# Kernel optimization log

Hardware: AMD Instinct MI355X
Metric: run time of the kernel (lower is better)

The kernel has to match this reference:

```python
import jax, jax.numpy as jnp
import numpy as np

N_NODES = 50000
N_EDGES = 500000
N_GRAPHS = 256
D_IN, D_H1, D_H2, D_H3, D_OUT = 768, 256, 128, 64, 2


def _glorot(key, shape):
    fan_in, fan_out = shape[1], shape[0]
    lim = float(np.sqrt(6.0 / (fan_in + fan_out)))
    return jax.random.uniform(key, shape, jnp.float32, -lim, lim)


def setup_inputs() -> dict:
    key = jax.random.key(0)
    ks = jax.random.split(key, 12)
    x = jax.random.normal(ks[0], (N_NODES, D_IN), jnp.float32)
    edge_index = jax.random.randint(ks[1], (2, N_EDGES), 0, N_NODES, jnp.int64)
    batch = jnp.sort(jax.random.randint(ks[2], (N_NODES,), 0, N_GRAPHS, jnp.int64))
    return {
        "x": x,
        "edge_index": edge_index,
        "batch": batch,
        # SAGEConv1: out = lin_l(mean_aggr) + lin_r(x); bias only on lin_l (PyG default)
        "W1_l": _glorot(ks[3], (D_H1, D_IN)),
        "b1_l": jnp.zeros((D_H1,), jnp.float32),
        "W1_r": _glorot(ks[4], (D_H1, D_IN)),
        # SAGEConv2
        "W2_l": _glorot(ks[5], (D_H2, D_H1)),
        "b2_l": jnp.zeros((D_H2,), jnp.float32),
        "W2_r": _glorot(ks[6], (D_H2, D_H1)),
        # MLP head
        "W3": _glorot(ks[7], (D_H3, D_H2)),
        "b3": jnp.zeros((D_H3,), jnp.float32),
        "W4": _glorot(ks[8], (D_OUT, D_H3)),
        "b4": jnp.zeros((D_OUT,), jnp.float32),
    }


def _sage_conv(x, src, dst, deg_inv, W_l, b_l, W_r):
    # mean aggregation of neighbor features: scatter-add then divide by in-degree
    aggr = jax.ops.segment_sum(x[src], dst, num_segments=N_NODES)  # [N, d]
    aggr = aggr * deg_inv[:, None]
    return aggr @ W_l.T + b_l + x @ W_r.T


def reference(x, edge_index, batch, W1_l, b1_l, W1_r, W2_l, b2_l, W2_r, W3, b3, W4, b4):
    src, dst = edge_index[0], edge_index[1]
    deg = jax.ops.segment_sum(jnp.ones((N_EDGES,), x.dtype), dst, num_segments=N_NODES)
    deg_inv = jnp.where(deg > 0, 1.0 / jnp.maximum(deg, 1.0), 0.0)

    h = jax.nn.relu(_sage_conv(x, src, dst, deg_inv, W1_l, b1_l, W1_r))
    h = jax.nn.relu(_sage_conv(h, src, dst, deg_inv, W2_l, b2_l, W2_r))

    # global_mean_pool over graph ids
    pooled = jax.ops.segment_sum(h, batch, num_segments=N_GRAPHS)  # [G, 128]
    cnt = jax.ops.segment_sum(jnp.ones((N_NODES,), h.dtype), batch, num_segments=N_GRAPHS)
    pooled = pooled / jnp.maximum(cnt, 1.0)[:, None]

    # dropout is identity in eval mode
    h = pooled @ W3.T + b3
    h = h @ W4.T + b4
    return jax.nn.softmax(h, axis=-1)
```

## Files before the change

kernel.cpp:

```cpp
#include <hip/hip_runtime.h>
#include <cstdint>
#include <cstddef>

#define N_NODES 50000
#define N_EDGES 500000
#define N_GRAPHS 256
#define D_IN 768
#define D_H1 256
#define D_H2 128

typedef __attribute__((ext_vector_type(8))) __bf16 bf16x8;
typedef __attribute__((ext_vector_type(4))) float f32x4;

__device__ __forceinline__ float bf2f(uint32_t u) {
    union { uint32_t i; float f; } v; v.i = u << 16; return v.f;
}
__device__ __forceinline__ uint32_t f2bf(float f) {
    union { float f; uint32_t i; } v; v.f = f;
    uint32_t u = v.i;
    return (u + 0x7FFFu + ((u >> 16) & 1u)) >> 16;
}

__global__ void k_packA(const float* __restrict__ in, uint16_t* __restrict__ out,
                        int nchunks, int KT, int K) {
    int c = blockIdx.x * 256 + threadIdx.x;
    if (c >= nchunks) return;
    int l = c & 63, t = c >> 6;
    int kt = t % KT, mt = t / KT;
    int fr = l & 15, fq = l >> 4;
    const float* p = in + (size_t)(mt * 16 + fr) * K + kt * 32 + fq * 8;
    float4 u = *(const float4*)p, v = *(const float4*)(p + 4);
    uint4 o;
    o.x = f2bf(u.x) | (f2bf(u.y) << 16);
    o.y = f2bf(u.z) | (f2bf(u.w) << 16);
    o.z = f2bf(v.x) | (f2bf(v.y) << 16);
    o.w = f2bf(v.z) | (f2bf(v.w) << 16);
    *(uint4*)(out + (size_t)c * 8) = o;
}

__global__ void k_packW(const float* __restrict__ inL, const float* __restrict__ inR,
                        uint16_t* __restrict__ out, int rowsL, int nchunks, int KT, int K) {
    int c = blockIdx.x * 256 + threadIdx.x;
    if (c >= nchunks) return;
    int l = c & 63, t = c >> 6;
    int kt = t % KT, mt = t / KT;
    int fr = l & 15, fq = l >> 4;
    int row = mt * 16 + fr;
    const float* src = (row < rowsL) ? (inL + (size_t)row * K) : (inR + (size_t)(row - rowsL) * K);
    const float* p = src + kt * 32 + fq * 8;
    float4 u = *(const float4*)p, v = *(const float4*)(p + 4);
    uint4 o;
    o.x = f2bf(u.x) | (f2bf(u.y) << 16);
    o.y = f2bf(u.z) | (f2bf(u.w) << 16);
    o.z = f2bf(v.x) | (f2bf(v.y) << 16);
    o.w = f2bf(v.z) | (f2bf(v.w) << 16);
    *(uint4*)(out + (size_t)c * 8) = o;
}

__global__ void k_hist(const int* __restrict__ dst, int* __restrict__ deg, int n) {
    int e = blockIdx.x * blockDim.x + threadIdx.x;
    if (e < n) atomicAdd(&deg[dst[e]], 1);
}

__global__ void k_scan1(const int* __restrict__ deg, int* __restrict__ row_ex,
                        int* __restrict__ bsum, int n) {
    __shared__ int buf[256];
    int t = threadIdx.x, i = blockIdx.x * 256 + t;
    int v = (i < n) ? deg[i] : 0;
    buf[t] = v; __syncthreads();
    for (int off = 1; off < 256; off <<= 1) {
        int u = (t >= off) ? buf[t - off] : 0;
        __syncthreads(); buf[t] += u; __syncthreads();
    }
    if (i < n) row_ex[i] = buf[t] - v;
    if (t == 255) bsum[blockIdx.x] = buf[255];
}
__global__ void k_scan2(const int* __restrict__ bsum, int* __restrict__ boff, int nb) {
    __shared__ int buf[256];
    int t = threadIdx.x;
    int v = (t < nb) ? bsum[t] : 0;
    buf[t] = v; __syncthreads();
    for (int off = 1; off < 256; off <<= 1) {
        int u = (t >= off) ? buf[t - off] : 0;
        __syncthreads(); buf[t] += u; __syncthreads();
    }
    if (t < nb) boff[t] = buf[t] - v;
}
__global__ void k_scan3(const int* __restrict__ deg, const int* __restrict__ boff,
                        int* __restrict__ row_start, float* __restrict__ deg_inv, int n) {
    int i = blockIdx.x * 256 + threadIdx.x;
    if (i < n) {
        row_start[i] += boff[blockIdx.x];
        int d = deg[i];
        deg_inv[i] = (d > 0) ? (1.0f / (float)d) : 0.0f;
    }
    if (blockIdx.x == 0 && threadIdx.x == 0) row_start[n] = N_EDGES;
}

__global__ void k_fill(const int* __restrict__ src, const int* __restrict__ dst,
                       const int* __restrict__ row_start, int* __restrict__ cursor,
                       int* __restrict__ csr_src, int n) {
    int e = blockIdx.x * blockDim.x + threadIdx.x;
    if (e < n) {
        int d = dst[e];
        int pos = row_start[d] + atomicAdd(&cursor[d], 1);
        csr_src[pos] = src[e];
    }
}

__global__ __launch_bounds__(256, 2) void k_mgemm(
    const uint16_t* __restrict__ Ap, const uint16_t* __restrict__ Bp,
    uint16_t* __restrict__ C, int M, int N, int KT)
{
    const int tid = threadIdx.x;
    const int wave = tid >> 6, lane = tid & 63;
    const int fr = lane & 15, fq = lane >> 4;
    const int bn = blockIdx.x * 256, bm = blockIdx.y * 128;
    const int wm = (wave >> 1) * 64, wn = (wave & 1) * 128;
    const int mtiles = (M + 15) >> 4;

    const bf16x8* ap[4];
    const bf16x8* bp[8];
    #pragma unroll
    for (int mi = 0; mi < 4; ++mi) {
        int mt = ((bm + wm) >> 4) + mi;
        if (mt > mtiles - 1) mt = mtiles - 1;
        ap[mi] = (const bf16x8*)Ap + (size_t)mt * KT * 64 + lane;
    }
    #pragma unroll
    for (int ni = 0; ni < 8; ++ni) {
        int nt = ((bn + wn) >> 4) + ni;
        bp[ni] = (const bf16x8*)Bp + (size_t)nt * KT * 64 + lane;
    }

    f32x4 acc[4][8] = {};
    bf16x8 a0[4], b0[8], a1[4], b1[8];

    auto lA = [&](int kt, bf16x8* d) {
        #pragma unroll
        for (int mi = 0; mi < 4; ++mi) d[mi] = ap[mi][kt * 64];
    };
    auto lB = [&](int kt, bf16x8* d) {
        #pragma unroll
        for (int ni = 0; ni < 8; ++ni) d[ni] = bp[ni][kt * 64];
    };
    auto step = [&](bf16x8* a, bf16x8* b) {
        #pragma unroll
        for (int mi = 0; mi < 4; ++mi)
            #pragma unroll
            for (int ni = 0; ni < 8; ++ni)
                acc[mi][ni] = __builtin_amdgcn_mfma_f32_16x16x32_bf16(
                    a[mi], b[ni], acc[mi][ni], 0, 0, 0);
    };

    lA(0, a0); lB(0, b0);
    for (int ks = 0; ks < KT; ks += 2) {
        lA(ks + 1, a1); lB(ks + 1, b1);
        step(a0, b0);
        if (ks + 2 < KT) { lA(ks + 2, a0); lB(ks + 2, b0); }
        step(a1, b1);
    }

    #pragma unroll
    for (int mi = 0; mi < 4; ++mi) {
        #pragma unroll
        for (int r = 0; r < 4; ++r) {
            int row = bm + wm + mi * 16 + fq * 4 + r;
            if (row >= M) continue;
            #pragma unroll
            for (int ni = 0; ni < 8; ++ni) {
                int col = bn + wn + ni * 16 + fr;
                C[(size_t)row * N + col] = (uint16_t)f2bf(acc[mi][ni][r]);
            }
        }
    }
}

__global__ __launch_bounds__(256) void k_agg1(
    const uint16_t* __restrict__ y, const int* __restrict__ row_start,
    const int* __restrict__ csr, const float* __restrict__ deg_inv,
    const float* __restrict__ bias, uint16_t* __restrict__ h1p)
{
    int node = blockIdx.x * 8 + (threadIdx.x >> 5);
    if (node >= N_NODES) return;
    int c = threadIdx.x & 31;
    int s = row_start[node], e = row_start[node + 1];
    float a[8] = {};
    int p = s;
    for (; p + 1 < e; p += 2) {
        uint4 t0 = *(const uint4*)(y + (size_t)csr[p] * 512 + c * 8);
        uint4 t1 = *(const uint4*)(y + (size_t)csr[p + 1] * 512 + c * 8);
        a[0] += bf2f(t0.x & 0xFFFF) + bf2f(t1.x & 0xFFFF);
        a[1] += bf2f(t0.x >> 16)    + bf2f(t1.x >> 16);
        a[2] += bf2f(t0.y & 0xFFFF) + bf2f(t1.y & 0xFFFF);
        a[3] += bf2f(t0.y >> 16)    + bf2f(t1.y >> 16);
        a[4] += bf2f(t0.z & 0xFFFF) + bf2f(t1.z & 0xFFFF);
        a[5] += bf2f(t0.z >> 16)    + bf2f(t1.z >> 16);
        a[6] += bf2f(t0.w & 0xFFFF) + bf2f(t1.w & 0xFFFF);
        a[7] += bf2f(t0.w >> 16)    + bf2f(t1.w >> 16);
    }
    if (p < e) {
        uint4 t0 = *(const uint4*)(y + (size_t)csr[p] * 512 + c * 8);
        a[0] += bf2f(t0.x & 0xFFFF); a[1] += bf2f(t0.x >> 16);
        a[2] += bf2f(t0.y & 0xFFFF); a[3] += bf2f(t0.y >> 16);
        a[4] += bf2f(t0.z & 0xFFFF); a[5] += bf2f(t0.z >> 16);
        a[6] += bf2f(t0.w & 0xFFFF); a[7] += bf2f(t0.w >> 16);
    }
    float w = deg_inv[node];
    uint4 tx = *(const uint4*)(y + (size_t)node * 512 + 256 + c * 8);
    float4 b0 = *(const float4*)(bias + c * 8);
    float4 b1 = *(const float4*)(bias + c * 8 + 4);
    float v0 = fmaxf(a[0] * w + bf2f(tx.x & 0xFFFF) + b0.x, 0.f);
    float v1 = fmaxf(a[1] * w + bf2f(tx.x >> 16)    + b0.y, 0.f);
    float v2 = fmaxf(a[2] * w + bf2f(tx.y & 0xFFFF) + b0.z, 0.f);
    float v3 = fmaxf(a[3] * w + bf2f(tx.y >> 16)    + b0.w, 0.f);
    float v4 = fmaxf(a[4] * w + bf2f(tx.z & 0xFFFF) + b1.x, 0.f);
    float v5 = fmaxf(a[5] * w + bf2f(tx.z >> 16)    + b1.y, 0.f);
    float v6 = fmaxf(a[6] * w + bf2f(tx.w & 0xFFFF) + b1.z, 0.f);
    float v7 = fmaxf(a[7] * w + bf2f(tx.w >> 16)    + b1.w, 0.f);
    uint4 o;
    o.x = f2bf(v0) | (f2bf(v1) << 16);
    o.y = f2bf(v2) | (f2bf(v3) << 16);
    o.z = f2bf(v4) | (f2bf(v5) << 16);
    o.w = f2bf(v6) | (f2bf(v7) << 16);
    uint32_t addr = (((node >> 4) * 8 + (c >> 2)) * 64 + (c & 3) * 16 + (node & 15));
    *(uint4*)(h1p + (size_t)addr * 8) = o;
}

__global__ __launch_bounds__(256) void k_agg2(
    const uint16_t* __restrict__ y, const int* __restrict__ row_start,
    const int* __restrict__ csr, const float* __restrict__ deg_inv,
    const float* __restrict__ bias, float* __restrict__ out)
{
    int node = blockIdx.x * 4 + (threadIdx.x >> 6);
    if (node >= N_NODES) return;
    int lane = threadIdx.x & 63;
    int s = row_start[node], e = row_start[node + 1];
    float a0 = 0.f, a1 = 0.f;
    int p = s;
    for (; p + 1 < e; p += 2) {
        uint32_t t0 = *(const uint32_t*)(y + (size_t)csr[p] * 256 + lane * 2);
        uint32_t t1 = *(const uint32_t*)(y + (size_t)csr[p + 1] * 256 + lane * 2);
        a0 += bf2f(t0 & 0xFFFF) + bf2f(t1 & 0xFFFF);
        a1 += bf2f(t0 >> 16)    + bf2f(t1 >> 16);
    }
    if (p < e) {
        uint32_t t0 = *(const uint32_t*)(y + (size_t)csr[p] * 256 + lane * 2);
        a0 += bf2f(t0 & 0xFFFF);
        a1 += bf2f(t0 >> 16);
    }
    float w = deg_inv[node];
    uint32_t tx = *(const uint32_t*)(y + (size_t)node * 256 + 128 + lane * 2);
    float2 b = *(const float2*)(bias + lane * 2);
    float2 o;
    o.x = fmaxf(a0 * w + bf2f(tx & 0xFFFF) + b.x, 0.f);
    o.y = fmaxf(a1 * w + bf2f(tx >> 16)    + b.y, 0.f);
    *(float2*)(out + (size_t)node * 128 + lane * 2) = o;
}

__global__ void k_pool(const float* __restrict__ h2, const int* __restrict__ batch,
                       float* __restrict__ pooled)
{
    int g = blockIdx.x;
    __shared__ int s_lo, s_hi;
    if (threadIdx.x == 0) {
        int lo = 0, hi = N_NODES;
        while (lo < hi) { int m = (lo + hi) >> 1; if (batch[m] < g) lo = m + 1; else hi = m; }
        s_lo = lo;
        int lo2 = lo, hi2 = N_NODES;
        while (lo2 < hi2) { int m = (lo2 + hi2) >> 1; if (batch[m] < g + 1) lo2 = m + 1; else hi2 = m; }
        s_hi = lo2;
    }
    __syncthreads();
    int dim = threadIdx.x;
    float sum = 0.f;
    for (int i = s_lo; i < s_hi; ++i) sum += h2[(size_t)i * D_H2 + dim];
    int cnt = s_hi - s_lo;
    pooled[g * D_H2 + dim] = sum / (float)(cnt > 0 ? cnt : 1);
}

__global__ void k_head(const float* __restrict__ pooled, const float* __restrict__ W3,
                       const float* __restrict__ b3, const float* __restrict__ W4,
                       const float* __restrict__ b4, float* __restrict__ out)
{
    int g = blockIdx.x;
    int j = threadIdx.x;
    __shared__ float p[128];
    __shared__ float hid[64];
    __shared__ float logit[2];
    p[j] = pooled[g * 128 + j];
    p[j + 64] = pooled[g * 128 + 64 + j];
    __syncthreads();
    float s = b3[j];
    #pragma unroll 4
    for (int k = 0; k < 128; ++k) s = fmaf(p[k], W3[j * 128 + k], s);
    hid[j] = s;
    __syncthreads();
    if (j < 2) {
        float l = b4[j];
        for (int k = 0; k < 64; ++k) l = fmaf(hid[k], W4[j * 64 + k], l);
        logit[j] = l;
    }
    __syncthreads();
    if (j == 0) {
        float m = fmaxf(logit[0], logit[1]);
        float e0 = expf(logit[0] - m), e1 = expf(logit[1] - m);
        float inv = 1.0f / (e0 + e1);
        out[g * 2 + 0] = e0 * inv;
        out[g * 2 + 1] = e1 * inv;
    }
}

extern "C" void kernel_launch(void* const* d_in, const int* in_sizes, int n_in,
                              void* d_out, int out_size, void* d_ws, size_t ws_size,
                              hipStream_t stream)
{
    const float* x     = (const float*)d_in[0];
    const int*   ei    = (const int*)d_in[1];
    const int*   batch = (const int*)d_in[2];
    const float* W1l   = (const float*)d_in[3];
    const float* b1l   = (const float*)d_in[4];
    const float* W1r   = (const float*)d_in[5];
    const float* W2l   = (const float*)d_in[6];
    const float* b2l   = (const float*)d_in[7];
    const float* W2r   = (const float*)d_in[8];
    const float* W3    = (const float*)d_in[9];
    const float* b3    = (const float*)d_in[10];
    const float* W4    = (const float*)d_in[11];
    const float* b4    = (const float*)d_in[12];
    float* out = (float*)d_out;

    const int* e_src = ei;
    const int* e_dst = ei + N_EDGES;

    char* ws = (char*)d_ws;
    size_t off = 0;
    auto alloc = [&](size_t bytes) -> void* {
        void* p = ws + off;
        off = (off + bytes + 255) & ~(size_t)255;
        return p;
    };
    int*      deg       = (int*)alloc((size_t)N_NODES * 4);
    int*      row_start = (int*)alloc((size_t)(N_NODES + 1) * 4);
    int*      cursor    = (int*)alloc((size_t)N_NODES * 4);
    int*      csr_src   = (int*)alloc((size_t)N_EDGES * 4);
    float*    deg_inv   = (float*)alloc((size_t)N_NODES * 4);
    int*      bsum      = (int*)alloc(256 * 4);
    int*      boff      = (int*)alloc(256 * 4);
    float*    pooled    = (float*)alloc((size_t)N_GRAPHS * D_H2 * 4);
    uint16_t* W1p       = (uint16_t*)alloc((size_t)512 * 768 * 2);
    uint16_t* W2p       = (uint16_t*)alloc((size_t)256 * 256 * 2);
    uint16_t* xp        = (uint16_t*)alloc((size_t)N_NODES * D_IN * 2);
    uint16_t* y1        = (uint16_t*)alloc((size_t)N_NODES * 512 * 2);
    uint16_t* h1p       = (uint16_t*)alloc((size_t)N_NODES * 256 * 2);

    uint16_t* y2 = xp;
    float*    h2 = (float*)(xp + (size_t)N_NODES * 256);

    hipMemsetAsync(deg, 0, (size_t)N_NODES * 4, stream);
    hipMemsetAsync(cursor, 0, (size_t)N_NODES * 4, stream);

    k_hist<<<(N_EDGES + 255) / 256, 256, 0, stream>>>(e_dst, deg, N_EDGES);
    int nscan = (N_NODES + 255) / 256;
    k_scan1<<<nscan, 256, 0, stream>>>(deg, row_start, bsum, N_NODES);
    k_scan2<<<1, 256, 0, stream>>>(bsum, boff, nscan);
    k_scan3<<<nscan, 256, 0, stream>>>(deg, boff, row_start, deg_inv, N_NODES);
    k_fill<<<(N_EDGES + 255) / 256, 256, 0, stream>>>(e_src, e_dst, row_start, cursor, csr_src, N_EDGES);

    int ncA = 3125 * 24 * 64;
    k_packA<<<(ncA + 255) / 256, 256, 0, stream>>>(x, xp, ncA, 24, 768);
    int ncW1 = 32 * 24 * 64;
    k_packW<<<(ncW1 + 255) / 256, 256, 0, stream>>>(W1l, W1r, W1p, 256, ncW1, 24, 768);
    int ncW2 = 16 * 8 * 64;
    k_packW<<<(ncW2 + 255) / 256, 256, 0, stream>>>(W2l, W2r, W2p, 128, ncW2, 8, 256);

    dim3 g1(2, (N_NODES + 127) / 128);
    k_mgemm<<<g1, 256, 0, stream>>>(xp, W1p, y1, N_NODES, 512, 24);
    k_agg1<<<(N_NODES + 7) / 8, 256, 0, stream>>>(y1, row_start, csr_src, deg_inv, b1l, h1p);

    dim3 g2(1, (N_NODES + 127) / 128);
    k_mgemm<<<g2, 256, 0, stream>>>(h1p, W2p, y2, N_NODES, 256, 8);
    k_agg2<<<(N_NODES + 3) / 4, 256, 0, stream>>>(y2, row_start, csr_src, deg_inv, b2l, h2);

    k_pool<<<N_GRAPHS, 128, 0, stream>>>(h2, batch, pooled);
    k_head<<<N_GRAPHS, 64, 0, stream>>>(pooled, W3, b3, W4, b4, out);
}
```

Baseline: 529.7 us.

## Fuse preprocessing kernels, use decoupled-lookback scan, fuse pooling into aggregation

Merges the x/W packing and the degree histogram into one multi-role kernel, replaces the three-kernel scan with a single-pass decoupled-lookback scan, and folds global mean pooling into the second aggregation via atomics. The mean division moves into the head kernel, and one memset now covers all zeroed buffers. This removes several launches and drops the h2 write and reread. The cost is float atomic contention on pooled, where one graph holds about 200 nodes, plus a lookback scan that depends on all its blocks being resident at once.

```diff
diff --git a/kernel.cpp b/kernel.cpp
--- a/kernel.cpp
+++ b/kernel.cpp
@@ -21,15 +21,9 @@
     return (u + 0x7FFFu + ((u >> 16) & 1u)) >> 16;
 }
 
-__global__ void k_packA(const float* __restrict__ in, uint16_t* __restrict__ out,
-                        int nchunks, int KT, int K) {
-    int c = blockIdx.x * 256 + threadIdx.x;
-    if (c >= nchunks) return;
-    int l = c & 63, t = c >> 6;
-    int kt = t % KT, mt = t / KT;
-    int fr = l & 15, fq = l >> 4;
-    const float* p = in + (size_t)(mt * 16 + fr) * K + kt * 32 + fq * 8;
-    float4 u = *(const float4*)p, v = *(const float4*)(p + 4);
+__device__ __forceinline__ void pack_chunk(const float* __restrict__ src_row,
+                                           uint16_t* __restrict__ out, int c) {
+    float4 u = *(const float4*)src_row, v = *(const float4*)(src_row + 4);
     uint4 o;
     o.x = f2bf(u.x) | (f2bf(u.y) << 16);
     o.y = f2bf(u.z) | (f2bf(u.w) << 16);
@@ -38,63 +32,85 @@
     *(uint4*)(out + (size_t)c * 8) = o;
 }
 
-__global__ void k_packW(const float* __restrict__ inL, const float* __restrict__ inR,
-                        uint16_t* __restrict__ out, int rowsL, int nchunks, int KT, int K) {
-    int c = blockIdx.x * 256 + threadIdx.x;
-    if (c >= nchunks) return;
-    int l = c & 63, t = c >> 6;
-    int kt = t % KT, mt = t / KT;
-    int fr = l & 15, fq = l >> 4;
-    int row = mt * 16 + fr;
-    const float* src = (row < rowsL) ? (inL + (size_t)row * K) : (inR + (size_t)(row - rowsL) * K);
-    const float* p = src + kt * 32 + fq * 8;
-    float4 u = *(const float4*)p, v = *(const float4*)(p + 4);
-    uint4 o;
-    o.x = f2bf(u.x) | (f2bf(u.y) << 16);
-    o.y = f2bf(u.z) | (f2bf(u.w) << 16);
-    o.z = f2bf(v.x) | (f2bf(v.y) << 16);
-    o.w = f2bf(v.z) | (f2bf(v.w) << 16);
-    *(uint4*)(out + (size_t)c * 8) = o;
-}
-
-__global__ void k_hist(const int* __restrict__ dst, int* __restrict__ deg, int n) {
-    int e = blockIdx.x * blockDim.x + threadIdx.x;
-    if (e < n) atomicAdd(&deg[dst[e]], 1);
-}
-
-__global__ void k_scan1(const int* __restrict__ deg, int* __restrict__ row_ex,
-                        int* __restrict__ bsum, int n) {
+#define PA_BLK 18750
+#define HI_BLK 1954
+#define PW1_BLK 192
+#define PW2_BLK 32
+__global__ __launch_bounds__(256) void k_combo(
+    const float* __restrict__ x, uint16_t* __restrict__ xp,
+    const int* __restrict__ dst, int* __restrict__ deg,
+    const float* __restrict__ W1l, const float* __restrict__ W1r, uint16_t* __restrict__ W1p,
+    const float* __restrict__ W2l, const float* __restrict__ W2r, uint16_t* __restrict__ W2p)
+{
+    int b = blockIdx.x, tid = threadIdx.x;
+    if (b < PA_BLK) {
+        int c = b * 256 + tid;
+        int l = c & 63, t = c >> 6;
+        int kt = t % 24, mt = t / 24;
+        int fr = l & 15, fq = l >> 4;
+        pack_chunk(x + (size_t)(mt * 16 + fr) * 768 + kt * 32 + fq * 8, xp, c);
+    } else if (b < PA_BLK + HI_BLK) {
+        int e = (b - PA_BLK) * 256 + tid;
+        if (e < N_EDGES) atomicAdd(&deg[dst[e]], 1);
+    } else if (b < PA_BLK + HI_BLK + PW1_BLK) {
+        int c = (b - PA_BLK - HI_BLK) * 256 + tid;
+        int l = c & 63, t = c >> 6;
+        int kt = t % 24, mt = t / 24;
+        int fr = l & 15, fq = l >> 4;
+        int row = mt * 16 + fr;
+        const float* src = (row < 256) ? (W1l + (size_t)row * 768)
+                                       : (W1r + (size_t)(row - 256) * 768);
+        pack_chunk(src + kt * 32 + fq * 8, W1p, c);
+    } else {
+        int c = (b - PA_BLK - HI_BLK - PW1_BLK) * 256 + tid;
+        int l = c & 63, t = c >> 6;
+        int kt = t % 8, mt = t / 8;
+        int fr = l & 15, fq = l >> 4;
+        int row = mt * 16 + fr;
+        const float* src = (row < 128) ? (W2l + (size_t)row * 256)
+                                       : (W2r + (size_t)(row - 128) * 256);
+        pack_chunk(src + kt * 32 + fq * 8, W2p, c);
+    }
+}
+
+__global__ __launch_bounds__(256) void k_scan(
+    const int* __restrict__ deg, unsigned long long* __restrict__ desc,
+    int* __restrict__ row_start, float* __restrict__ deg_inv, int n)
+{
     __shared__ int buf[256];
-    int t = threadIdx.x, i = blockIdx.x * 256 + t;
+    __shared__ int s_prefix;
+    int bid = blockIdx.x, t = threadIdx.x;
+    int i = bid * 256 + t;
     int v = (i < n) ? deg[i] : 0;
     buf[t] = v; __syncthreads();
     for (int off = 1; off < 256; off <<= 1) {
         int u = (t >= off) ? buf[t - off] : 0;
         __syncthreads(); buf[t] += u; __syncthreads();
     }
-    if (i < n) row_ex[i] = buf[t] - v;
-    if (t == 255) bsum[blockIdx.x] = buf[255];
-}
-__global__ void k_scan2(const int* __restrict__ bsum, int* __restrict__ boff, int nb) {
-    __shared__ int buf[256];
-    int t = threadIdx.x;
-    int v = (t < nb) ? bsum[t] : 0;
-    buf[t] = v; __syncthreads();
-    for (int off = 1; off < 256; off <<= 1) {
-        int u = (t >= off) ? buf[t - off] : 0;
-        __syncthreads(); buf[t] += u; __syncthreads();
-    }
-    if (t < nb) boff[t] = buf[t] - v;
-}
-__global__ void k_scan3(const int* __restrict__ deg, const int* __restrict__ boff,
-                        int* __restrict__ row_start, float* __restrict__ deg_inv, int n) {
-    int i = blockIdx.x * 256 + threadIdx.x;
+    if (t == 0) {
+        unsigned long long total = (unsigned long long)(unsigned)buf[255];
+        __hip_atomic_store(&desc[bid], (1ull << 32) | total,
+                           __ATOMIC_RELEASE, __HIP_MEMORY_SCOPE_AGENT);
+        unsigned long long run = 0;
+        for (int j = bid - 1; j >= 0; --j) {
+            unsigned long long d;
+            do {
+                d = __hip_atomic_load(&desc[j], __ATOMIC_ACQUIRE, __HIP_MEMORY_SCOPE_AGENT);
+            } while ((d >> 32) == 0);
+            run += (d & 0xFFFFFFFFull);
+            if ((d >> 32) == 2) break;
+        }
+        __hip_atomic_store(&desc[bid], (2ull << 32) | (run + total),
+                           __ATOMIC_RELEASE, __HIP_MEMORY_SCOPE_AGENT);
+        s_prefix = (int)run;
+    }
+    __syncthreads();
+    int ex = s_prefix + buf[t] - v;
     if (i < n) {
-        row_start[i] += boff[blockIdx.x];
-        int d = deg[i];
-        deg_inv[i] = (d > 0) ? (1.0f / (float)d) : 0.0f;
-    }
-    if (blockIdx.x == 0 && threadIdx.x == 0) row_start[n] = N_EDGES;
+        row_start[i] = ex;
+        deg_inv[i] = (v > 0) ? (1.0f / (float)v) : 0.0f;
+        if (i == n - 1) row_start[n] = ex + v;
+    }
 }
 
 __global__ void k_fill(const int* __restrict__ src, const int* __restrict__ dst,
@@ -227,10 +243,11 @@
     *(uint4*)(h1p + (size_t)addr * 8) = o;
 }
 
-__global__ __launch_bounds__(256) void k_agg2(
+__global__ __launch_bounds__(256) void k_agg2pool(
     const uint16_t* __restrict__ y, const int* __restrict__ row_start,
     const int* __restrict__ csr, const float* __restrict__ deg_inv,
-    const float* __restrict__ bias, float* __restrict__ out)
+    const float* __restrict__ bias, const int* __restrict__ batch,
+    float* __restrict__ pooled)
 {
     int node = blockIdx.x * 4 + (threadIdx.x >> 6);
     if (node >= N_NODES) return;
@@ -252,44 +269,35 @@
     float w = deg_inv[node];
     uint32_t tx = *(const uint32_t*)(y + (size_t)node * 256 + 128 + lane * 2);
     float2 b = *(const float2*)(bias + lane * 2);
-    float2 o;
-    o.x = fmaxf(a0 * w + bf2f(tx & 0xFFFF) + b.x, 0.f);
-    o.y = fmaxf(a1 * w + bf2f(tx >> 16)    + b.y, 0.f);
-    *(float2*)(out + (size_t)node * 128 + lane * 2) = o;
-}
-
-__global__ void k_pool(const float* __restrict__ h2, const int* __restrict__ batch,
-                       float* __restrict__ pooled)
-{
-    int g = blockIdx.x;
-    __shared__ int s_lo, s_hi;
-    if (threadIdx.x == 0) {
-        int lo = 0, hi = N_NODES;
-        while (lo < hi) { int m = (lo + hi) >> 1; if (batch[m] < g) lo = m + 1; else hi = m; }
-        s_lo = lo;
-        int lo2 = lo, hi2 = N_NODES;
-        while (lo2 < hi2) { int m = (lo2 + hi2) >> 1; if (batch[m] < g + 1) lo2 = m + 1; else hi2 = m; }
-        s_hi = lo2;
-    }
-    __syncthreads();
-    int dim = threadIdx.x;
-    float sum = 0.f;
-    for (int i = s_lo; i < s_hi; ++i) sum += h2[(size_t)i * D_H2 + dim];
-    int cnt = s_hi - s_lo;
-    pooled[g * D_H2 + dim] = sum / (float)(cnt > 0 ? cnt : 1);
-}
-
-__global__ void k_head(const float* __restrict__ pooled, const float* __restrict__ W3,
-                       const float* __restrict__ b3, const float* __restrict__ W4,
-                       const float* __restrict__ b4, float* __restrict__ out)
+    float h0 = fmaxf(a0 * w + bf2f(tx & 0xFFFF) + b.x, 0.f);
+    float h1 = fmaxf(a1 * w + bf2f(tx >> 16)    + b.y, 0.f);
+    int g = batch[node];
+    atomicAdd(&pooled[g * 128 + lane * 2], h0);
+    atomicAdd(&pooled[g * 128 + lane * 2 + 1], h1);
+}
+
+__global__ void k_head(const float* __restrict__ pooled, const int* __restrict__ batch,
+                       const float* __restrict__ W3, const float* __restrict__ b3,
+                       const float* __restrict__ W4, const float* __restrict__ b4,
+                       float* __restrict__ out)
 {
     int g = blockIdx.x;
     int j = threadIdx.x;
     __shared__ float p[128];
     __shared__ float hid[64];
     __shared__ float logit[2];
-    p[j] = pooled[g * 128 + j];
-    p[j + 64] = pooled[g * 128 + 64 + j];
+    __shared__ float s_inv;
+    if (j == 0) {
+        int lo = 0, hi = N_NODES;
+        while (lo < hi) { int m = (lo + hi) >> 1; if (batch[m] < g) lo = m + 1; else hi = m; }
+        int lo2 = lo, hi2 = N_NODES;
+        while (lo2 < hi2) { int m = (lo2 + hi2) >> 1; if (batch[m] < g + 1) lo2 = m + 1; else hi2 = m; }
+        int cnt = lo2 - lo;
+        s_inv = 1.0f / (float)(cnt > 0 ? cnt : 1);
+    }
+    __syncthreads();
+    p[j]      = pooled[g * 128 + j] * s_inv;
+    p[j + 64] = pooled[g * 128 + 64 + j] * s_inv;
     __syncthreads();
     float s = b3[j];
     #pragma unroll 4
@@ -341,13 +349,13 @@
         return p;
     };
     int*      deg       = (int*)alloc((size_t)N_NODES * 4);
+    int*      cursor    = (int*)alloc((size_t)N_NODES * 4);
+    float*    pooled    = (float*)alloc((size_t)N_GRAPHS * D_H2 * 4);
+    unsigned long long* desc = (unsigned long long*)alloc(196 * 8);
+    size_t zero_span = off;
     int*      row_start = (int*)alloc((size_t)(N_NODES + 1) * 4);
-    int*      cursor    = (int*)alloc((size_t)N_NODES * 4);
     int*      csr_src   = (int*)alloc((size_t)N_EDGES * 4);
     float*    deg_inv   = (float*)alloc((size_t)N_NODES * 4);
-    int*      bsum      = (int*)alloc(256 * 4);
-    int*      boff      = (int*)alloc(256 * 4);
-    float*    pooled    = (float*)alloc((size_t)N_GRAPHS * D_H2 * 4);
     uint16_t* W1p       = (uint16_t*)alloc((size_t)512 * 768 * 2);
     uint16_t* W2p       = (uint16_t*)alloc((size_t)256 * 256 * 2);
     uint16_t* xp        = (uint16_t*)alloc((size_t)N_NODES * D_IN * 2);
@@ -355,33 +363,18 @@
     uint16_t* h1p       = (uint16_t*)alloc((size_t)N_NODES * 256 * 2);
 
     uint16_t* y2 = xp;
-    float*    h2 = (float*)(xp + (size_t)N_NODES * 256);
-
-    hipMemsetAsync(deg, 0, (size_t)N_NODES * 4, stream);
-    hipMemsetAsync(cursor, 0, (size_t)N_NODES * 4, stream);
-
-    k_hist<<<(N_EDGES + 255) / 256, 256, 0, stream>>>(e_dst, deg, N_EDGES);
-    int nscan = (N_NODES + 255) / 256;
-    k_scan1<<<nscan, 256, 0, stream>>>(deg, row_start, bsum, N_NODES);
-    k_scan2<<<1, 256, 0, stream>>>(bsum, boff, nscan);
-    k_scan3<<<nscan, 256, 0, stream>>>(deg, boff, row_start, deg_inv, N_NODES);
+
+    hipMemsetAsync(deg, 0, zero_span, stream);
+
+    k_combo<<<PA_BLK + HI_BLK + PW1_BLK + PW2_BLK, 256, 0, stream>>>(
+        x, xp, e_dst, deg, W1l, W1r, W1p, W2l, W2r, W2p);
+    k_scan<<<196, 256, 0, stream>>>(deg, desc, row_start, deg_inv, N_NODES);
     k_fill<<<(N_EDGES + 255) / 256, 256, 0, stream>>>(e_src, e_dst, row_start, cursor, csr_src, N_EDGES);
-
-    int ncA = 3125 * 24 * 64;
-    k_packA<<<(ncA + 255) / 256, 256, 0, stream>>>(x, xp, ncA, 24, 768);
-    int ncW1 = 32 * 24 * 64;
-    k_packW<<<(ncW1 + 255) / 256, 256, 0, stream>>>(W1l, W1r, W1p, 256, ncW1, 24, 768);
-    int ncW2 = 16 * 8 * 64;
-    k_packW<<<(ncW2 + 255) / 256, 256, 0, stream>>>(W2l, W2r, W2p, 128, ncW2, 8, 256);
-
     dim3 g1(2, (N_NODES + 127) / 128);
     k_mgemm<<<g1, 256, 0, stream>>>(xp, W1p, y1, N_NODES, 512, 24);
     k_agg1<<<(N_NODES + 7) / 8, 256, 0, stream>>>(y1, row_start, csr_src, deg_inv, b1l, h1p);
-
     dim3 g2(1, (N_NODES + 127) / 128);
     k_mgemm<<<g2, 256, 0, stream>>>(h1p, W2p, y2, N_NODES, 256, 8);
-    k_agg2<<<(N_NODES + 3) / 4, 256, 0, stream>>>(y2, row_start, csr_src, deg_inv, b2l, h2);
-
-    k_pool<<<N_GRAPHS, 128, 0, stream>>>(h2, batch, pooled);
-    k_head<<<N_GRAPHS, 64, 0, stream>>>(pooled, W3, b3, W4, b4, out);
-}
+    k_agg2pool<<<(N_NODES + 3) / 4, 256, 0, stream>>>(y2, row_start, csr_src, deg_inv, b2l, batch, pooled);
+    k_head<<<N_GRAPHS, 64, 0, stream>>>(pooled, batch, W3, b3, W4, b4, out);
+}
```

Result: no change. 531.3 us (+0.3%).
